# Performance work log

Hardware: AMD Instinct MI355X
Metric: run time of the kernel (lower is better)

## Reference

```python
import jax, jax.numpy as jnp
import numpy as np
import math

B, N, C = 4, 4096, 1024
H, K_LM = 16, 256
HEAD_DIM = C // H


def setup_inputs() -> dict:
    key = jax.random.key(0)
    k1, k2, k3, k4, k5 = jax.random.split(key, 5)
    x = jax.random.normal(k1, (B, N, C), dtype=jnp.float32)
    Wqkv = jax.random.normal(k2, (3 * C, C), dtype=jnp.float32) * 0.02
    E = jax.random.normal(k3, (H, K_LM, N), dtype=jnp.float32) * 0.02
    Wproj = jax.random.normal(k4, (C, C), dtype=jnp.float32) * 0.02
    bproj = jax.random.normal(k5, (C,), dtype=jnp.float32) * 0.02
    return {"x": x, "Wqkv": Wqkv, "E": E, "Wproj": Wproj, "bproj": bproj}


def reference(x, Wqkv, E, Wproj, bproj):
    Bsz, n, c = x.shape
    h, d = H, c // H
    # qkv projection (no bias): [B,N,3C] -> (3,B,H,N,d)
    qkv = (x @ Wqkv.T).reshape(Bsz, n, 3, h, d).transpose(2, 0, 3, 1, 4)
    q, k, v = qkv[0], qkv[1], qkv[2]
    # Linformer landmark projection: E[h,k,n] @ K/V[b,h,n,d] -> [b,h,k,d]
    k_lm = jnp.einsum('hkn,bhnd->bhkd', E, k)
    v_lm = jnp.einsum('hkn,bhnd->bhkd', E, v)
    # scaled dot + softmax over landmarks: [b,h,n,k]
    dot = jnp.einsum('bhnd,bhkd->bhnk', q, k_lm) / math.sqrt(d)
    attn = jax.nn.softmax(dot, axis=-1)
    # weighted sum; faithful to original: reshape (B,H,N,d) -> (B,N,C) WITHOUT head transpose
    out = jnp.einsum('bhnk,bhkd->bhnd', attn, v_lm).reshape(Bsz, n, c)
    # output projection (dropouts are identity at eval / p=0)
    return out @ Wproj.T + bproj
```

## Files before the change

### kernel.cpp

```cpp
#include <hip/hip_runtime.h>


typedef unsigned short ushort_t;
typedef float f32x4 __attribute__((ext_vector_type(4)));
typedef __bf16 bf16x8 __attribute__((ext_vector_type(8)));
typedef unsigned short ushort8 __attribute__((ext_vector_type(8)));
typedef unsigned short ushort4_t __attribute__((ext_vector_type(4)));

__device__ inline ushort_t f2bf(float f) {
  unsigned int u = __float_as_uint(f);
  u += 0x7fff + ((u >> 16) & 1);
  return (ushort_t)(u >> 16);
}

__device__ inline void gload_lds16(const ushort_t* g, ushort_t* l) {
  __builtin_amdgcn_global_load_lds(
      (const __attribute__((address_space(1))) void*)g,
      (__attribute__((address_space(3))) void*)l, 16, 0, 0);
}

__global__ __launch_bounds__(256) void cvt_all(
    const float* __restrict__ x,  ushort_t* __restrict__ xo,
    const float* __restrict__ w1, ushort_t* __restrict__ w1o,
    const float* __restrict__ e,  ushort_t* __restrict__ eo,
    const float* __restrict__ w2, ushort_t* __restrict__ w2o) {
  int i = blockIdx.x * blockDim.x + threadIdx.x;
  const float* in; ushort_t* out; int idx;
  if (i < 4194304)               { in = x;  out = xo;  idx = i; }
  else if (i < 4980736)          { in = w1; out = w1o; idx = i - 4194304; }
  else if (i < 9175040)          { in = e;  out = eo;  idx = i - 4980736; }
  else                           { in = w2; out = w2o; idx = i - 9175040; }
  float4 v = ((const float4*)in)[idx];
  ushort4_t o;
  o.x = f2bf(v.x); o.y = f2bf(v.y); o.z = f2bf(v.z); o.w = f2bf(v.w);
  ((ushort4_t*)out)[idx] = o;
}

__device__ inline void swizzle_tiles(int tiles_n, int& mt, int& nt) {
  const int lin = blockIdx.y * gridDim.x + blockIdx.x;
  const int g = lin >> 7, r = lin & 127;
  const int ngrp = tiles_n >> 3;
  const int gn = g % ngrp, gm = g / ngrp;
  mt = gm * 16 + (r & 15);
  nt = gn * 8 + (r >> 4);
}

__global__ __launch_bounds__(256) void gemm_qkv(
    const ushort_t* __restrict__ A, const ushort_t* __restrict__ W,
    ushort_t* __restrict__ q, ushort_t* __restrict__ kT, ushort_t* __restrict__ vT) {
  __shared__ __align__(16) ushort_t smem[17408];
  const int tid = threadIdx.x, lane = tid & 63, w = tid >> 6;
  const int wm = w & 1, wn = w >> 1;
  const int l15 = lane & 15, quad = lane >> 4;
  int mt, nt;
  swizzle_tiles(24, mt, nt);
  const long long m0 = (long long)mt * 128;
  const long long n0 = (long long)nt * 128;
  const int K = 1024;

  const f32x4 zz = {0.f, 0.f, 0.f, 0.f};
  f32x4 acc[4][4];
#pragma unroll
  for (int i = 0; i < 4; i++)
#pragma unroll
    for (int j = 0; j < 4; j++) acc[i][j] = zz;

  const int lr = lane >> 2, lc = (lane & 3) * 8;
  const ushort_t* gA0 = A + (m0 + 32 * w + lr) * K + lc;
  const ushort_t* gB0 = W + (n0 + 32 * w + lr) * K + lc;
  ushort_t* lA0 = smem + 32 * w * 32;
  ushort_t* lB0 = smem + 8192 + 32 * w * 32;

  for (int k0 = 0; k0 < K; k0 += 64) {
    __syncthreads();
#pragma unroll
    for (int p = 0; p < 2; p++) {
#pragma unroll
      for (int j = 0; j < 2; j++) {
        gload_lds16(gA0 + k0 + 32 * p + 16 * j * K, lA0 + p * 4096 + j * 512);
        gload_lds16(gB0 + k0 + 32 * p + 16 * j * K, lB0 + p * 4096 + j * 512);
      }
    }
    __syncthreads();
#pragma unroll
    for (int p = 0; p < 2; p++) {
      bf16x8 af[4], bf[4];
#pragma unroll
      for (int i = 0; i < 4; i++)
        af[i] = *(const bf16x8*)(smem + p * 4096 + (wm * 64 + i * 16 + l15) * 32 + quad * 8);
#pragma unroll
      for (int j = 0; j < 4; j++)
        bf[j] = *(const bf16x8*)(smem + 8192 + p * 4096 + (wn * 64 + j * 16 + l15) * 32 + quad * 8);
#pragma unroll
      for (int i = 0; i < 4; i++)
#pragma unroll
        for (int j = 0; j < 4; j++)
          acc[i][j] = __builtin_amdgcn_mfma_f32_16x16x32_bf16(af[i], bf[j], acc[i][j], 0, 0, 0);
    }
  }

  const int b     = (int)(m0 >> 12);
  const int nrow0 = (int)(m0 & 4095);
  const int s     = (int)(n0 >> 10);
  const int h0    = (int)((n0 & 1023) >> 6);

  if (s == 0) {
#pragma unroll
    for (int i = 0; i < 4; i++)
#pragma unroll
      for (int j = 0; j < 4; j++) {
        int c  = wn * 64 + j * 16;
        int h  = h0 + (c >> 6);
        int dd = (c & 63) + l15;
        long long z = b * 16 + h;
        int nb = nrow0 + wm * 64 + i * 16 + quad * 4;
#pragma unroll
        for (int r = 0; r < 4; r++)
          q[z * 262144 + (long long)(nb + r) * 64 + dd] = f2bf(acc[i][j][r]);
      }
  } else {
    ushort_t (*T)[136] = (ushort_t(*)[136])smem;
    __syncthreads();
#pragma unroll
    for (int i = 0; i < 4; i++)
#pragma unroll
      for (int j = 0; j < 4; j++) {
        int c = wn * 64 + j * 16 + l15;
        int t = wm * 64 + i * 16 + quad * 4;
        ushort4_t o = {f2bf(acc[i][j][0]), f2bf(acc[i][j][1]),
                       f2bf(acc[i][j][2]), f2bf(acc[i][j][3])};
        *(ushort4_t*)(&T[c][t]) = o;
      }
    __syncthreads();
    ushort_t* KV = (s == 1) ? kT : vT;
#pragma unroll
    for (int it = 0; it < 8; it++) {
      int ch = it * 256 + tid;
      int cl = ch >> 4, tc = (ch & 15) * 8;
      ushort8 v = *(const ushort8*)(&T[cl][tc]);
      int h = h0 + (cl >> 6), dd = cl & 63;
      long long z = b * 16 + h;
      *(ushort8*)(KV + z * 262144 + (long long)dd * 4096 + nrow0 + tc) = v;
    }
  }
}

__global__ __launch_bounds__(256) void lm_gemm(
    const ushort_t* __restrict__ E, const ushort_t* __restrict__ kT,
    const ushort_t* __restrict__ vT, float* __restrict__ pK, float* __restrict__ pV) {
  __shared__ __align__(16) ushort_t smem[12288];
  const int tid = threadIdx.x, lane = tid & 63, w = tid >> 6;
  const int l15 = lane & 15, quad = lane >> 4;
  const int kt = blockIdx.x;
  const int s  = blockIdx.y;
  const int z  = blockIdx.z;
  const int h  = z & 15;
  const int lr = lane >> 2, lc = (lane & 3) * 8;

  const ushort_t* gE = E  + ((long long)h * 256 + kt * 64 + 16 * w + lr) * 4096 + s * 1024 + lc;
  const ushort_t* gK = kT + ((long long)z * 64 + 16 * w + lr) * 4096 + s * 1024 + lc;
  const ushort_t* gV = vT + ((long long)z * 64 + 16 * w + lr) * 4096 + s * 1024 + lc;
  ushort_t* lE = smem + 512 * w;
  ushort_t* lK = smem + 4096 + 512 * w;
  ushort_t* lV = smem + 8192 + 512 * w;

  const f32x4 zz = {0.f, 0.f, 0.f, 0.f};
  f32x4 aK[4], aV[4];
#pragma unroll
  for (int j = 0; j < 4; j++) { aK[j] = zz; aV[j] = zz; }

  for (int n = 0; n < 1024; n += 64) {
    __syncthreads();
#pragma unroll
    for (int p = 0; p < 2; p++) {
      gload_lds16(gE + n + 32 * p, lE + p * 2048);
      gload_lds16(gK + n + 32 * p, lK + p * 2048);
      gload_lds16(gV + n + 32 * p, lV + p * 2048);
    }
    __syncthreads();
#pragma unroll
    for (int p = 0; p < 2; p++) {
      bf16x8 ef = *(const bf16x8*)(smem + p * 2048 + (w * 16 + l15) * 32 + quad * 8);
#pragma unroll
      for (int j = 0; j < 4; j++) {
        bf16x8 kf = *(const bf16x8*)(smem + 4096 + p * 2048 + (j * 16 + l15) * 32 + quad * 8);
        aK[j] = __builtin_amdgcn_mfma_f32_16x16x32_bf16(ef, kf, aK[j], 0, 0, 0);
        bf16x8 vf = *(const bf16x8*)(smem + 8192 + p * 2048 + (j * 16 + l15) * 32 + quad * 8);
        aV[j] = __builtin_amdgcn_mfma_f32_16x16x32_bf16(ef, vf, aV[j], 0, 0, 0);
      }
    }
  }

  float* oK = pK + ((long long)(z * 4 + s) * 256 + kt * 64) * 64;
  float* oV = pV + ((long long)(z * 4 + s) * 256 + kt * 64) * 64;
#pragma unroll
  for (int j = 0; j < 4; j++)
#pragma unroll
    for (int r = 0; r < 4; r++) {
      int row = w * 16 + quad * 4 + r, col = j * 16 + l15;
      oK[row * 64 + col] = aK[j][r];
      oV[row * 64 + col] = aV[j][r];
    }
}

__global__ __launch_bounds__(256) void lm_reduce(
    const float* __restrict__ pK, const float* __restrict__ pV,
    ushort_t* __restrict__ klm, ushort_t* __restrict__ vlmT) {
  __shared__ float Tv[64][68];
  const int tid = threadIdx.x;
  const int kt = blockIdx.x;
  const int z  = blockIdx.y;
  const long long base = (long long)z * 4 * 16384 + kt * 64 * 64;
  const int row = tid >> 2, c0 = (tid & 3) * 16;

  float sk[16];
#pragma unroll
  for (int g = 0; g < 4; g++) {
    f32x4 a = {0.f, 0.f, 0.f, 0.f};
#pragma unroll
    for (int s = 0; s < 4; s++)
      a += *(const f32x4*)(pK + base + (long long)s * 16384 + row * 64 + c0 + g * 4);
    sk[g * 4 + 0] = a[0]; sk[g * 4 + 1] = a[1]; sk[g * 4 + 2] = a[2]; sk[g * 4 + 3] = a[3];
  }
  {
    ushort_t* dst = klm + ((long long)z * 256 + kt * 64 + row) * 64 + c0;
    ushort8 o0, o1;
#pragma unroll
    for (int i = 0; i < 8; i++) { o0[i] = f2bf(sk[i]); o1[i] = f2bf(sk[8 + i]); }
    *(ushort8*)(dst) = o0;
    *(ushort8*)(dst + 8) = o1;
  }

#pragma unroll
  for (int g = 0; g < 4; g++) {
    f32x4 a = {0.f, 0.f, 0.f, 0.f};
#pragma unroll
    for (int s = 0; s < 4; s++)
      a += *(const f32x4*)(pV + base + (long long)s * 16384 + row * 64 + c0 + g * 4);
    *(f32x4*)(&Tv[row][c0 + g * 4]) = a;
  }
  __syncthreads();
  {
    ushort8 o0, o1;
#pragma unroll
    for (int i = 0; i < 8; i++) {
      o0[i] = f2bf(Tv[c0 + i][row]);
      o1[i] = f2bf(Tv[c0 + 8 + i][row]);
    }
    ushort_t* dst = vlmT + ((long long)z * 64 + row) * 256 + kt * 64 + c0;
    *(ushort8*)(dst) = o0;
    *(ushort8*)(dst + 8) = o1;
  }
}

__global__ __launch_bounds__(256) void attn_fused(
    const ushort_t* __restrict__ Q, const ushort_t* __restrict__ Klm,
    const ushort_t* __restrict__ VlmT, ushort_t* __restrict__ O) {
  __shared__ __align__(16) ushort_t smem[16896];
  ushort_t (*As)[40]  = (ushort_t(*)[40])smem;
  ushort_t (*Bs)[40]  = (ushort_t(*)[40])(smem + 2560);
  ushort_t (*P)[264]  = (ushort_t(*)[264])smem;
  const int tid = threadIdx.x, lane = tid & 63, w = tid >> 6;
  const int l15 = lane & 15, quad = lane >> 4;
  const int z = blockIdx.z;
  const long long m0 = (long long)blockIdx.x * 64;
  const ushort_t* Qb = Q + (long long)z * 262144;
  const ushort_t* Kb = Klm + (long long)z * 16384;
  const ushort_t* Vb = VlmT + (long long)z * 16384;

  const f32x4 zz = {0.f, 0.f, 0.f, 0.f};
  f32x4 acc[16];
#pragma unroll
  for (int j = 0; j < 16; j++) acc[j] = zz;

  const int sr = tid >> 2, sc = (tid & 3) * 8;

  for (int kt = 0; kt < 2; kt++) {
    const int k0 = kt * 32;
    ushort8 av = *(const ushort8*)(Qb + (m0 + sr) * 64 + k0 + sc);
    ushort8 bv[4];
#pragma unroll
    for (int r = 0; r < 4; r++) {
      int c = r * 256 + tid;
      bv[r] = *(const ushort8*)(Kb + (c >> 2) * 64 + k0 + (c & 3) * 8);
    }
    __syncthreads();
    *(ushort8*)(&As[sr][sc]) = av;
#pragma unroll
    for (int r = 0; r < 4; r++) {
      int c = r * 256 + tid;
      *(ushort8*)(&Bs[c >> 2][(c & 3) * 8]) = bv[r];
    }
    __syncthreads();
    bf16x8 af = *(const bf16x8*)(&As[w * 16 + l15][quad * 8]);
#pragma unroll
    for (int j = 0; j < 16; j++) {
      bf16x8 bfj = *(const bf16x8*)(&Bs[j * 16 + l15][quad * 8]);
      acc[j] = __builtin_amdgcn_mfma_f32_16x16x32_bf16(af, bfj, acc[j], 0, 0, 0);
    }
  }

  __syncthreads();
#pragma unroll
  for (int r = 0; r < 4; r++) {
    float x[16];
    float vmax = -1e30f;
#pragma unroll
    for (int j = 0; j < 16; j++) { x[j] = acc[j][r] * 0.125f; vmax = fmaxf(vmax, x[j]); }
#pragma unroll
    for (int m = 1; m < 16; m <<= 1) vmax = fmaxf(vmax, __shfl_xor(vmax, m, 64));
    float s = 0.f;
#pragma unroll
    for (int j = 0; j < 16; j++) { x[j] = __expf(x[j] - vmax); s += x[j]; }
#pragma unroll
    for (int m = 1; m < 16; m <<= 1) s += __shfl_xor(s, m, 64);
    float inv = 1.0f / s;
    int row = w * 16 + quad * 4 + r;
#pragma unroll
    for (int j = 0; j < 16; j++)
      P[row][j * 16 + l15] = f2bf(x[j] * inv);
  }
  __syncthreads();

  f32x4 o_acc[4];
#pragma unroll
  for (int j = 0; j < 4; j++) o_acc[j] = zz;
#pragma unroll
  for (int kc = 0; kc < 8; kc++) {
    bf16x8 pf = *(const bf16x8*)(&P[w * 16 + l15][kc * 32 + quad * 8]);
#pragma unroll
    for (int j = 0; j < 4; j++) {
      bf16x8 vf = *(const bf16x8*)(Vb + (j * 16 + l15) * 256 + kc * 32 + quad * 8);
      o_acc[j] = __builtin_amdgcn_mfma_f32_16x16x32_bf16(pf, vf, o_acc[j], 0, 0, 0);
    }
  }

#pragma unroll
  for (int j = 0; j < 4; j++)
#pragma unroll
    for (int r = 0; r < 4; r++) {
      int row = w * 16 + quad * 4 + r;
      int col = j * 16 + l15;
      O[(long long)z * 262144 + (m0 + row) * 64 + col] = f2bf(o_acc[j][r]);
    }
}

__global__ __launch_bounds__(256) void gemm_nt_128(
    const ushort_t* __restrict__ A, const ushort_t* __restrict__ B,
    float* __restrict__ C, const float* __restrict__ bias,
    int M, int N, int K) {
  __shared__ __align__(16) ushort_t smem[16384];
  const int tid = threadIdx.x, lane = tid & 63, w = tid >> 6;
  const int wm = w & 1, wn = w >> 1;
  const int l15 = lane & 15, quad = lane >> 4;
  int mt, nt;
  swizzle_tiles(gridDim.y, mt, nt);
  const long long m0 = (long long)mt * 128;
  const long long n0 = (long long)nt * 128;

  const f32x4 zz = {0.f, 0.f, 0.f, 0.f};
  f32x4 acc[4][4];
#pragma unroll
  for (int i = 0; i < 4; i++)
#pragma unroll
    for (int j = 0; j < 4; j++) acc[i][j] = zz;

  const int lr = lane >> 2, lc = (lane & 3) * 8;
  const ushort_t* gA0 = A + (m0 + 32 * w + lr) * K + lc;
  const ushort_t* gB0 = B + (n0 + 32 * w + lr) * K + lc;
  ushort_t* lA0 = smem + 32 * w * 32;
  ushort_t* lB0 = smem + 8192 + 32 * w * 32;

  for (int k0 = 0; k0 < K; k0 += 64) {
    __syncthreads();
#pragma unroll
    for (int p = 0; p < 2; p++) {
#pragma unroll
      for (int j = 0; j < 2; j++) {
        gload_lds16(gA0 + k0 + 32 * p + 16 * j * K, lA0 + p * 4096 + j * 512);
        gload_lds16(gB0 + k0 + 32 * p + 16 * j * K, lB0 + p * 4096 + j * 512);
      }
    }
    __syncthreads();
#pragma unroll
    for (int p = 0; p < 2; p++) {
      bf16x8 af[4], bf[4];
#pragma unroll
      for (int i = 0; i < 4; i++)
        af[i] = *(const bf16x8*)(smem + p * 4096 + (wm * 64 + i * 16 + l15) * 32 + quad * 8);
#pragma unroll
      for (int j = 0; j < 4; j++)
        bf[j] = *(const bf16x8*)(smem + 8192 + p * 4096 + (wn * 64 + j * 16 + l15) * 32 + quad * 8);
#pragma unroll
      for (int i = 0; i < 4; i++)
#pragma unroll
        for (int j = 0; j < 4; j++)
          acc[i][j] = __builtin_amdgcn_mfma_f32_16x16x32_bf16(af[i], bf[j], acc[i][j], 0, 0, 0);
    }
  }

#pragma unroll
  for (int i = 0; i < 4; i++)
#pragma unroll
    for (int j = 0; j < 4; j++) {
      long long row = m0 + wm * 64 + i * 16 + quad * 4;
      long long col = n0 + wn * 64 + j * 16 + l15;
      float bv = bias ? bias[col] : 0.0f;
#pragma unroll
      for (int r = 0; r < 4; r++)
        C[(row + r) * (long long)N + col] = acc[i][j][r] + bv;
    }
}

extern "C" void kernel_launch(void* const* d_in, const int* in_sizes, int n_in,
                              void* d_out, int out_size, void* d_ws, size_t ws_size,
                              hipStream_t stream) {
  const float* x     = (const float*)d_in[0];
  const float* Wqkv  = (const float*)d_in[1];
  const float* E     = (const float*)d_in[2];
  const float* Wproj = (const float*)d_in[3];
  const float* bproj = (const float*)d_in[4];
  float* out = (float*)d_out;

  char* ws = (char*)d_ws;
  ushort_t* x_bf     = (ushort_t*)(ws + 0);
  float*    pK       = (float*)   (ws + 0);
  float*    pV       = (float*)   (ws + 16777216);
  ushort_t* wqkv_bf  = (ushort_t*)(ws + 33554432);
  ushort_t* e_bf     = (ushort_t*)(ws + 39845888);
  ushort_t* wproj_bf = (ushort_t*)(ws + 73400320);
  ushort_t* q_bf     = (ushort_t*)(ws + 75497472);
  ushort_t* kT       = (ushort_t*)(ws + 109051904);
  ushort_t* vT       = (ushort_t*)(ws + 142606336);
  ushort_t* klm      = (ushort_t*)(ws + 176160768);
  ushort_t* vlmT     = (ushort_t*)(ws + 178257920);

  cvt_all<<<36864, 256, 0, stream>>>(x, x_bf, Wqkv, wqkv_bf, E, e_bf, Wproj, wproj_bf);

  gemm_qkv<<<dim3(128, 24), 256, 0, stream>>>(x_bf, wqkv_bf, q_bf, kT, vT);

  lm_gemm<<<dim3(4, 4, 64), 256, 0, stream>>>(e_bf, kT, vT, pK, pV);

  lm_reduce<<<dim3(4, 64), 256, 0, stream>>>(pK, pV, klm, vlmT);

  attn_fused<<<dim3(64, 1, 64), 256, 0, stream>>>(q_bf, klm, vlmT, x_bf);

  gemm_nt_128<<<dim3(128, 8), 256, 0, stream>>>(x_bf, wproj_bf, out, bproj, 16384, 1024, 1024);
}
```

Before: 486.0 us.

## Replace 128x128 GEMMs with pipelined 256x256 double-buffered swizzled-LDS GEMM core

Both the QKV projection and the output projection now use a shared 256x256-tile, 512-thread GEMM core. It double-buffers LDS with direct global-to-LDS loads, XOR-swizzles LDS to avoid bank conflicts, and interleaves quarter-tile MFMA phases with prefetch using explicit waitcnt, barriers and setprio. Blocks are remapped so that neighbouring tiles land on the same XCD, and the K/V transpose epilogue is split into two halves. The aim is more data reuse per tile and overlap of memory with MFMA. The cost is 128KB of LDS per block, which gives one block per CU, and fewer blocks in total (256 for the output projection).

```diff
diff --git a/kernel.cpp b/kernel.cpp
--- a/kernel.cpp
+++ b/kernel.cpp
@@ -36,111 +36,178 @@
   ((ushort4_t*)out)[idx] = o;
 }
 
-__device__ inline void swizzle_tiles(int tiles_n, int& mt, int& nt) {
-  const int lin = blockIdx.y * gridDim.x + blockIdx.x;
-  const int g = lin >> 7, r = lin & 127;
-  const int ngrp = tiles_n >> 3;
-  const int gn = g % ngrp, gm = g / ngrp;
-  mt = gm * 16 + (r & 15);
-  nt = gn * 8 + (r >> 4);
-}
-
-__global__ __launch_bounds__(256) void gemm_qkv(
+
+#define BARX __builtin_amdgcn_s_barrier()
+#define WVM(n) do { asm volatile("s_waitcnt vmcnt(" #n ")" ::: "memory"); \
+                    __builtin_amdgcn_sched_barrier(0); } while (0)
+#define WLG  do { asm volatile("s_waitcnt lgkmcnt(0)" ::: "memory"); \
+                  __builtin_amdgcn_sched_barrier(0); } while (0)
+
+#define STG_A(h, slot, tt) do { \
+    gload_lds16(sA[h][0] + (tt) * 64, (ushort_t*)(smem + (slot) * 32768 + (h) * 16384 + (w * 2 + 0) * 1024)); \
+    gload_lds16(sA[h][1] + (tt) * 64, (ushort_t*)(smem + (slot) * 32768 + (h) * 16384 + (w * 2 + 1) * 1024)); \
+  } while (0)
+#define STG_B(h, slot, tt) do { \
+    gload_lds16(sB[h][0] + (tt) * 64, (ushort_t*)(smem + 65536 + (slot) * 32768 + (h) * 16384 + (w * 2 + 0) * 1024)); \
+    gload_lds16(sB[h][1] + (tt) * 64, (ushort_t*)(smem + 65536 + (slot) * 32768 + (h) * 16384 + (w * 2 + 1) * 1024)); \
+  } while (0)
+
+#define RD_A(mh) do { \
+    const char* ba_ = smem + sl * 32768 + ((mh) * 128 + wm * 64 + l15) * 128; \
+    _Pragma("unroll") for (int i_ = 0; i_ < 4; i_++) { \
+      aF[i_][0] = *(const bf16x8*)(ba_ + i_ * 2048 + cs0); \
+      aF[i_][1] = *(const bf16x8*)(ba_ + i_ * 2048 + cs1); } \
+  } while (0)
+#define RD_B(nh) do { \
+    const char* bb_ = smem + 65536 + sl * 32768 + ((nh) * 128 + wn * 32 + l15) * 128; \
+    _Pragma("unroll") for (int j_ = 0; j_ < 2; j_++) { \
+      bF[j_][0] = *(const bf16x8*)(bb_ + j_ * 2048 + cs0); \
+      bF[j_][1] = *(const bf16x8*)(bb_ + j_ * 2048 + cs1); } \
+  } while (0)
+
+#define MQ(mh, nh) do { \
+    _Pragma("unroll") for (int i_ = 0; i_ < 4; i_++) \
+    _Pragma("unroll") for (int j_ = 0; j_ < 2; j_++) { \
+      acc[(mh) * 4 + i_][(nh) * 2 + j_] = __builtin_amdgcn_mfma_f32_16x16x32_bf16( \
+          aF[i_][0], bF[j_][0], acc[(mh) * 4 + i_][(nh) * 2 + j_], 0, 0, 0); \
+      acc[(mh) * 4 + i_][(nh) * 2 + j_] = __builtin_amdgcn_mfma_f32_16x16x32_bf16( \
+          aF[i_][1], bF[j_][1], acc[(mh) * 4 + i_][(nh) * 2 + j_], 0, 0, 0); } \
+  } while (0)
+
+__device__ __attribute__((always_inline)) inline void pipe256(
+    const ushort_t* __restrict__ Ag, const ushort_t* __restrict__ Bg,
+    long long m0, long long n0, char* smem, f32x4 acc[8][4]) {
+  const int tid = threadIdx.x, lane = tid & 63, w = tid >> 6;
+  const int l15 = lane & 15, quad = lane >> 4;
+  const int wm = w >> 2, wn = w & 3;
+  const int sw = l15 & 7;
+  const int K = 1024;
+  const int cs0 = ((0 * 4 + quad) ^ sw) << 4;
+  const int cs1 = ((1 * 4 + quad) ^ sw) << 4;
+  const int lr8 = lane >> 3;
+  const int sdat = ((lane & 7) ^ lr8) * 8;
+  const ushort_t* sA[2][2];
+  const ushort_t* sB[2][2];
+#pragma unroll
+  for (int h = 0; h < 2; h++)
+#pragma unroll
+    for (int q = 0; q < 2; q++) {
+      sA[h][q] = Ag + (m0 + h * 128 + (w * 2 + q) * 8 + lr8) * K + sdat;
+      sB[h][q] = Bg + (n0 + h * 128 + (w * 2 + q) * 8 + lr8) * K + sdat;
+    }
+
+  const f32x4 zz = {0.f, 0.f, 0.f, 0.f};
+#pragma unroll
+  for (int i = 0; i < 8; i++)
+#pragma unroll
+    for (int j = 0; j < 4; j++) acc[i][j] = zz;
+
+  bf16x8 aF[4][2];
+  bf16x8 bF[2][2];
+
+  STG_A(0, 0, 0); STG_B(0, 0, 0); STG_A(1, 0, 0); STG_B(1, 0, 0);
+  WVM(4);
+  BARX;
+
+#pragma unroll 2
+  for (int t = 0; t < 16; ++t) {
+    const int sl = t & 1, sn = sl ^ 1;
+    const bool pf = (t < 15);
+    RD_A(0); RD_B(0);
+    if (pf) STG_A(0, sn, t + 1);
+    BARX; WLG;
+    __builtin_amdgcn_s_setprio(1); MQ(0, 0); __builtin_amdgcn_s_setprio(0);
+    if (pf) { WVM(4); } else { WVM(2); }
+    BARX;
+    RD_A(1);
+    if (pf) STG_B(0, sn, t + 1);
+    BARX; WLG;
+    __builtin_amdgcn_s_setprio(1); MQ(1, 0); __builtin_amdgcn_s_setprio(0);
+    if (pf) { WVM(4); } else { WVM(0); }
+    BARX;
+    RD_B(1);
+    if (pf) STG_A(1, sn, t + 1);
+    BARX; WLG;
+    __builtin_amdgcn_s_setprio(1); MQ(1, 1); __builtin_amdgcn_s_setprio(0);
+    BARX;
+    RD_A(0);
+    if (pf) STG_B(1, sn, t + 1);
+    BARX; WLG;
+    __builtin_amdgcn_s_setprio(1); MQ(0, 1); __builtin_amdgcn_s_setprio(0);
+    if (pf) WVM(4);
+    BARX;
+  }
+}
+
+__global__ __launch_bounds__(512) void gemm_qkv(
     const ushort_t* __restrict__ A, const ushort_t* __restrict__ W,
     ushort_t* __restrict__ q, ushort_t* __restrict__ kT, ushort_t* __restrict__ vT) {
-  __shared__ __align__(16) ushort_t smem[17408];
+  __shared__ __align__(16) char smem[131072];
+  const int lin = blockIdx.x;
+  const int xcd = lin & 7, rr_ = lin >> 3;
+  const int mt = xcd * 8 + (rr_ & 7);
+  const int nt = rr_ >> 3;
+  const long long m0 = (long long)mt * 256;
+  const long long n0 = (long long)nt * 256;
+
+  f32x4 acc[8][4];
+  pipe256(A, W, m0, n0, smem, acc);
+
   const int tid = threadIdx.x, lane = tid & 63, w = tid >> 6;
-  const int wm = w & 1, wn = w >> 1;
   const int l15 = lane & 15, quad = lane >> 4;
-  int mt, nt;
-  swizzle_tiles(24, mt, nt);
-  const long long m0 = (long long)mt * 128;
-  const long long n0 = (long long)nt * 128;
-  const int K = 1024;
-
-  const f32x4 zz = {0.f, 0.f, 0.f, 0.f};
-  f32x4 acc[4][4];
-#pragma unroll
-  for (int i = 0; i < 4; i++)
-#pragma unroll
-    for (int j = 0; j < 4; j++) acc[i][j] = zz;
-
-  const int lr = lane >> 2, lc = (lane & 3) * 8;
-  const ushort_t* gA0 = A + (m0 + 32 * w + lr) * K + lc;
-  const ushort_t* gB0 = W + (n0 + 32 * w + lr) * K + lc;
-  ushort_t* lA0 = smem + 32 * w * 32;
-  ushort_t* lB0 = smem + 8192 + 32 * w * 32;
-
-  for (int k0 = 0; k0 < K; k0 += 64) {
-    __syncthreads();
-#pragma unroll
-    for (int p = 0; p < 2; p++) {
-#pragma unroll
-      for (int j = 0; j < 2; j++) {
-        gload_lds16(gA0 + k0 + 32 * p + 16 * j * K, lA0 + p * 4096 + j * 512);
-        gload_lds16(gB0 + k0 + 32 * p + 16 * j * K, lB0 + p * 4096 + j * 512);
-      }
-    }
-    __syncthreads();
-#pragma unroll
-    for (int p = 0; p < 2; p++) {
-      bf16x8 af[4], bf[4];
-#pragma unroll
-      for (int i = 0; i < 4; i++)
-        af[i] = *(const bf16x8*)(smem + p * 4096 + (wm * 64 + i * 16 + l15) * 32 + quad * 8);
-#pragma unroll
-      for (int j = 0; j < 4; j++)
-        bf[j] = *(const bf16x8*)(smem + 8192 + p * 4096 + (wn * 64 + j * 16 + l15) * 32 + quad * 8);
-#pragma unroll
-      for (int i = 0; i < 4; i++)
-#pragma unroll
-        for (int j = 0; j < 4; j++)
-          acc[i][j] = __builtin_amdgcn_mfma_f32_16x16x32_bf16(af[i], bf[j], acc[i][j], 0, 0, 0);
-    }
-  }
-
+  const int wm = w >> 2, wn = w & 3;
   const int b     = (int)(m0 >> 12);
   const int nrow0 = (int)(m0 & 4095);
   const int s     = (int)(n0 >> 10);
-  const int h0    = (int)((n0 & 1023) >> 6);
+  const int ncol0 = (int)(n0 & 1023);
+  const int h0    = ncol0 >> 6;
 
   if (s == 0) {
 #pragma unroll
-    for (int i = 0; i < 4; i++)
-#pragma unroll
-      for (int j = 0; j < 4; j++) {
-        int c  = wn * 64 + j * 16;
-        int h  = h0 + (c >> 6);
-        int dd = (c & 63) + l15;
-        long long z = b * 16 + h;
-        int nb = nrow0 + wm * 64 + i * 16 + quad * 4;
-#pragma unroll
-        for (int r = 0; r < 4; r++)
-          q[z * 262144 + (long long)(nb + r) * 64 + dd] = f2bf(acc[i][j][r]);
-      }
+    for (int mh = 0; mh < 2; mh++)
+#pragma unroll
+      for (int i = 0; i < 4; i++)
+#pragma unroll
+        for (int nh = 0; nh < 2; nh++)
+#pragma unroll
+          for (int j = 0; j < 2; j++) {
+            int cx = ncol0 + nh * 128 + wn * 32 + j * 16;
+            int h  = cx >> 6;
+            int dd = (cx & 63) + l15;
+            long long z = (long long)b * 16 + h;
+            int nb = nrow0 + mh * 128 + wm * 64 + i * 16 + quad * 4;
+#pragma unroll
+            for (int r = 0; r < 4; r++)
+              q[z * 262144 + (long long)(nb + r) * 64 + dd] = f2bf(acc[mh * 4 + i][nh * 2 + j][r]);
+          }
   } else {
     ushort_t (*T)[136] = (ushort_t(*)[136])smem;
-    __syncthreads();
-#pragma unroll
-    for (int i = 0; i < 4; i++)
-#pragma unroll
-      for (int j = 0; j < 4; j++) {
-        int c = wn * 64 + j * 16 + l15;
-        int t = wm * 64 + i * 16 + quad * 4;
-        ushort4_t o = {f2bf(acc[i][j][0]), f2bf(acc[i][j][1]),
-                       f2bf(acc[i][j][2]), f2bf(acc[i][j][3])};
-        *(ushort4_t*)(&T[c][t]) = o;
+    ushort_t* KV = (s == 1) ? kT : vT;
+#pragma unroll
+    for (int p = 0; p < 2; p++) {
+      __syncthreads();
+#pragma unroll
+      for (int i = 0; i < 4; i++)
+#pragma unroll
+        for (int nh = 0; nh < 2; nh++)
+#pragma unroll
+          for (int j = 0; j < 2; j++) {
+            int c = nh * 128 + wn * 32 + j * 16 + l15;
+            int t = wm * 64 + i * 16 + quad * 4;
+            ushort4_t o = {f2bf(acc[p * 4 + i][nh * 2 + j][0]), f2bf(acc[p * 4 + i][nh * 2 + j][1]),
+                           f2bf(acc[p * 4 + i][nh * 2 + j][2]), f2bf(acc[p * 4 + i][nh * 2 + j][3])};
+            *(ushort4_t*)(&T[c][t]) = o;
+          }
+      __syncthreads();
+#pragma unroll
+      for (int it = 0; it < 8; it++) {
+        int ch = it * 512 + tid;
+        int cl = ch >> 4, tc = (ch & 15) * 8;
+        ushort8 v = *(const ushort8*)(&T[cl][tc]);
+        int h = h0 + (cl >> 6), dd = cl & 63;
+        long long z = (long long)b * 16 + h;
+        *(ushort8*)(KV + z * 262144 + (long long)dd * 4096 + (nrow0 + p * 128 + tc)) = v;
       }
-    __syncthreads();
-    ushort_t* KV = (s == 1) ? kT : vT;
-#pragma unroll
-    for (int it = 0; it < 8; it++) {
-      int ch = it * 256 + tid;
-      int cl = ch >> 4, tc = (ch & 15) * 8;
-      ushort8 v = *(const ushort8*)(&T[cl][tc]);
-      int h = h0 + (cl >> 6), dd = cl & 63;
-      long long z = b * 16 + h;
-      *(ushort8*)(KV + z * 262144 + (long long)dd * 4096 + nrow0 + tc) = v;
     }
   }
 }
@@ -345,71 +412,39 @@
     }
 }
 
-__global__ __launch_bounds__(256) void gemm_nt_128(
+__global__ __launch_bounds__(512) void gemm_nt_256(
     const ushort_t* __restrict__ A, const ushort_t* __restrict__ B,
-    float* __restrict__ C, const float* __restrict__ bias,
-    int M, int N, int K) {
-  __shared__ __align__(16) ushort_t smem[16384];
+    float* __restrict__ C, const float* __restrict__ bias) {
+  __shared__ __align__(16) char smem[131072];
+  const int lin = blockIdx.x;
+  const int xcd = lin & 7, rr_ = lin >> 3;
+  const int mt = xcd * 8 + (rr_ & 7);
+  const int nt = rr_ >> 3;
+  const long long m0 = (long long)mt * 256;
+  const long long n0 = (long long)nt * 256;
+
+  f32x4 acc[8][4];
+  pipe256(A, B, m0, n0, smem, acc);
+
   const int tid = threadIdx.x, lane = tid & 63, w = tid >> 6;
-  const int wm = w & 1, wn = w >> 1;
   const int l15 = lane & 15, quad = lane >> 4;
-  int mt, nt;
-  swizzle_tiles(gridDim.y, mt, nt);
-  const long long m0 = (long long)mt * 128;
-  const long long n0 = (long long)nt * 128;
-
-  const f32x4 zz = {0.f, 0.f, 0.f, 0.f};
-  f32x4 acc[4][4];
-#pragma unroll
-  for (int i = 0; i < 4; i++)
-#pragma unroll
-    for (int j = 0; j < 4; j++) acc[i][j] = zz;
-
-  const int lr = lane >> 2, lc = (lane & 3) * 8;
-  const ushort_t* gA0 = A + (m0 + 32 * w + lr) * K + lc;
-  const ushort_t* gB0 = B + (n0 + 32 * w + lr) * K + lc;
-  ushort_t* lA0 = smem + 32 * w * 32;
-  ushort_t* lB0 = smem + 8192 + 32 * w * 32;
-
-  for (int k0 = 0; k0 < K; k0 += 64) {
-    __syncthreads();
-#pragma unroll
-    for (int p = 0; p < 2; p++) {
-#pragma unroll
-      for (int j = 0; j < 2; j++) {
-        gload_lds16(gA0 + k0 + 32 * p + 16 * j * K, lA0 + p * 4096 + j * 512);
-        gload_lds16(gB0 + k0 + 32 * p + 16 * j * K, lB0 + p * 4096 + j * 512);
-      }
-    }
-    __syncthreads();
-#pragma unroll
-    for (int p = 0; p < 2; p++) {
-      bf16x8 af[4], bf[4];
-#pragma unroll
-      for (int i = 0; i < 4; i++)
-        af[i] = *(const bf16x8*)(smem + p * 4096 + (wm * 64 + i * 16 + l15) * 32 + quad * 8);
-#pragma unroll
-      for (int j = 0; j < 4; j++)
-        bf[j] = *(const bf16x8*)(smem + 8192 + p * 4096 + (wn * 64 + j * 16 + l15) * 32 + quad * 8);
-#pragma unroll
-      for (int i = 0; i < 4; i++)
-#pragma unroll
-        for (int j = 0; j < 4; j++)
-          acc[i][j] = __builtin_amdgcn_mfma_f32_16x16x32_bf16(af[i], bf[j], acc[i][j], 0, 0, 0);
-    }
-  }
-
-#pragma unroll
-  for (int i = 0; i < 4; i++)
-#pragma unroll
-    for (int j = 0; j < 4; j++) {
-      long long row = m0 + wm * 64 + i * 16 + quad * 4;
-      long long col = n0 + wn * 64 + j * 16 + l15;
-      float bv = bias ? bias[col] : 0.0f;
-#pragma unroll
-      for (int r = 0; r < 4; r++)
-        C[(row + r) * (long long)N + col] = acc[i][j][r] + bv;
-    }
+  const int wm = w >> 2, wn = w & 3;
+
+#pragma unroll
+  for (int mh = 0; mh < 2; mh++)
+#pragma unroll
+    for (int i = 0; i < 4; i++)
+#pragma unroll
+      for (int nh = 0; nh < 2; nh++)
+#pragma unroll
+        for (int j = 0; j < 2; j++) {
+          long long row = m0 + mh * 128 + wm * 64 + i * 16 + quad * 4;
+          long long col = n0 + nh * 128 + wn * 32 + j * 16 + l15;
+          float bv = bias[col];
+#pragma unroll
+          for (int r = 0; r < 4; r++)
+            C[(row + r) * 1024 + col] = acc[mh * 4 + i][nh * 2 + j][r] + bv;
+        }
 }
 
 extern "C" void kernel_launch(void* const* d_in, const int* in_sizes, int n_in,
@@ -437,7 +472,7 @@
 
   cvt_all<<<36864, 256, 0, stream>>>(x, x_bf, Wqkv, wqkv_bf, E, e_bf, Wproj, wproj_bf);
 
-  gemm_qkv<<<dim3(128, 24), 256, 0, stream>>>(x_bf, wqkv_bf, q_bf, kT, vT);
+  gemm_qkv<<<768, 512, 0, stream>>>(x_bf, wqkv_bf, q_bf, kT, vT);
 
   lm_gemm<<<dim3(4, 4, 64), 256, 0, stream>>>(e_bf, kT, vT, pK, pV);
 
@@ -445,5 +480,5 @@
 
   attn_fused<<<dim3(64, 1, 64), 256, 0, stream>>>(q_bf, klm, vlmT, x_bf);
 
-  gemm_nt_128<<<dim3(128, 8), 256, 0, stream>>>(x_bf, wproj_bf, out, bproj, 16384, 1024, 1024);
-}
+  gemm_nt_256<<<256, 512, 0, stream>>>(x_bf, wproj_bf, out, bproj);
+}
```

Measured after the change: 451.8 us. 7.0% less time.
